# Kernel optimization log

Measured on AMD Instinct MI355X. Metric: run time of the kernel, lower is better.

Reference implementation:

```python
import jax, jax.numpy as jnp
import numpy as np

B, C, H, W = 64, 96, 56, 56
KS = 7
HIDDEN = 512
EPS = 1e-5


def setup_inputs() -> dict:
    key = jax.random.key(0)
    k1, k2, k3 = jax.random.split(key, 3)
    hw = H * W
    return {
        "x": jax.random.normal(k1, (B, C, H, W), dtype=jnp.float32),
        "ln_gamma": jnp.ones((hw,), jnp.float32),
        "ln_beta": jnp.zeros((hw,), jnp.float32),
        "w0": jax.random.normal(k2, (hw, HIDDEN), jnp.float32) * 0.02,
        "b0": jnp.zeros((HIDDEN,), jnp.float32),
        "w1": jax.random.normal(k3, (HIDDEN, KS * KS), jnp.float32) * 0.02,
        "b1": jnp.zeros((KS * KS,), jnp.float32),
        "attn_bias": jnp.zeros((B * C,), jnp.float32),
    }


def reference(x, ln_gamma, ln_beta, w0, b0, w1, b1, attn_bias):
    b, c, h, w = x.shape
    a = x.reshape(b, c, h * w)  # B C (HW)
    # LayerNorm over flattened spatial dim
    mu = jnp.mean(a, axis=-1, keepdims=True)
    var = jnp.mean(jnp.square(a - mu), axis=-1, keepdims=True)
    a = (a - mu) * jax.lax.rsqrt(var + EPS) * ln_gamma + ln_beta
    # 2-layer MLP -> per-(B,C) KxK kernel; exact GELU matches torch nn.GELU()
    a = jax.nn.gelu(jnp.einsum("bcn,nd->bcd", a, w0) + b0, approximate=False)
    a = jnp.einsum("bcd,dk->bck", a, w1) + b1  # (B, C, K*K)
    weight = a.reshape(b * c, 1, KS, KS)  # OIHW, one input channel per group
    xin = x.reshape(1, b * c, h, w)
    pad = KS // 2
    out = jax.lax.conv_general_dilated(
        xin, weight,
        window_strides=(1, 1),
        padding=[(pad, pad), (pad, pad)],
        dimension_numbers=("NCHW", "OIHW", "NCHW"),
        feature_group_count=b * c,
    )
    out = out + attn_bias.reshape(1, b * c, 1, 1)
    return out.reshape(b, c, h, w)
```

## Files before the change

### kernel.cpp

```cpp
#include <hip/hip_runtime.h>
#include <hip/hip_bf16.h>

#define BB 64
#define CC 96
#define HH 56
#define WW 56
#define HWS 3136
#define BC 6144
#define HIDDEN 512
#define KS 7
#define KK2 49
#define K1 3136
#define N1 512
#define EPS 1e-5f

typedef __attribute__((ext_vector_type(8))) short short8;
typedef __attribute__((ext_vector_type(4))) float f32x4;

static __device__ __forceinline__ unsigned short f2bf(float f) {
    union { float f; unsigned int u; } un; un.f = f;
    unsigned int r = un.u + 0x7fffu + ((un.u >> 16) & 1u);
    return (unsigned short)(r >> 16);
}

__global__ __launch_bounds__(256) void ln_kernel(const float* __restrict__ x,
                                                 const float* __restrict__ gamma,
                                                 const float* __restrict__ beta,
                                                 unsigned short* __restrict__ a) {
    const int row = blockIdx.x;
    const float4* xr = (const float4*)(x + (size_t)row * HWS);
    float sum = 0.f, sq = 0.f;
    for (int i = threadIdx.x; i < HWS / 4; i += 256) {
        float4 v = xr[i];
        sum += (v.x + v.y) + (v.z + v.w);
        sq = fmaf(v.x, v.x, sq); sq = fmaf(v.y, v.y, sq);
        sq = fmaf(v.z, v.z, sq); sq = fmaf(v.w, v.w, sq);
    }
    #pragma unroll
    for (int off = 32; off > 0; off >>= 1) {
        sum += __shfl_down(sum, off, 64);
        sq  += __shfl_down(sq,  off, 64);
    }
    __shared__ float s1[4], s2[4];
    const int lane = threadIdx.x & 63, wave = threadIdx.x >> 6;
    if (lane == 0) { s1[wave] = sum; s2[wave] = sq; }
    __syncthreads();
    sum = s1[0] + s1[1] + s1[2] + s1[3];
    sq  = s2[0] + s2[1] + s2[2] + s2[3];
    const float mu = sum * (1.f / HWS);
    const float var = fmaf(-mu, mu, sq * (1.f / HWS));
    const float rs = rsqrtf(var + EPS);
    const float4* gr = (const float4*)gamma;
    const float4* br = (const float4*)beta;
    ushort4* ar = (ushort4*)(a + (size_t)row * HWS);
    for (int i = threadIdx.x; i < HWS / 4; i += 256) {
        float4 v = xr[i], g = gr[i], b = br[i];
        ushort4 o;
        o.x = f2bf((v.x - mu) * rs * g.x + b.x);
        o.y = f2bf((v.y - mu) * rs * g.y + b.y);
        o.z = f2bf((v.z - mu) * rs * g.z + b.z);
        o.w = f2bf((v.w - mu) * rs * g.w + b.w);
        ar[i] = o;
    }
}

__global__ __launch_bounds__(256) void w0t_kernel(const float* __restrict__ w0,
                                                  unsigned short* __restrict__ w0t) {
    __shared__ float tile[64][65];
    const int kb = blockIdx.x * 64;
    const int nb = blockIdx.y * 64;
    for (int i = threadIdx.x; i < 64 * 64; i += 256) {
        int r = i >> 6, c = i & 63;
        tile[r][c] = w0[(size_t)(kb + r) * N1 + nb + c];
    }
    __syncthreads();
    for (int i = threadIdx.x; i < 64 * 64; i += 256) {
        int r = i >> 6, c = i & 63;
        w0t[(size_t)(nb + r) * K1 + kb + c] = f2bf(tile[c][r]);
    }
}

__global__ __launch_bounds__(256) void gemm1_kernel(const unsigned short* __restrict__ A,
                                                    const unsigned short* __restrict__ Bt,
                                                    const float* __restrict__ b0,
                                                    float* __restrict__ hidden) {
    __shared__ __align__(16) char smem[32768];
    const int t = threadIdx.x;
    const int wave = t >> 6, lane = t & 63;
    const int wm = wave >> 1, wn = wave & 1;
    const int tm = blockIdx.x * 64;
    const int tn = blockIdx.y * 64;

    f32x4 acc[2][2] = {};

    auto stage = [&](int buf, int k0) {
        #pragma unroll
        for (int it = 0; it < 2; ++it) {
            int chunk = it * 256 + t;
            int row = chunk >> 3;
            int cb = (chunk & 7) << 4;
            int sb = cb ^ ((row & 7) << 4);
            const char* gA = (const char*)(A + (size_t)(tm + row) * K1 + k0) + sb;
            const char* gB = (const char*)(Bt + (size_t)(tn + row) * K1 + k0) + sb;
            char* ldsA = smem + buf * 16384 + it * 4096 + wave * 1024;
            char* ldsB = smem + buf * 16384 + 8192 + it * 4096 + wave * 1024;
            __builtin_amdgcn_global_load_lds(
                (const __attribute__((address_space(1))) unsigned int*)gA,
                (__attribute__((address_space(3))) unsigned int*)ldsA, 16, 0, 0);
            __builtin_amdgcn_global_load_lds(
                (const __attribute__((address_space(1))) unsigned int*)gB,
                (__attribute__((address_space(3))) unsigned int*)ldsB, 16, 0, 0);
        }
    };

    auto compute = [&](int buf) {
        const char* base = smem + buf * 16384;
        #pragma unroll
        for (int kk = 0; kk < 2; ++kk) {
            short8 af[2], bfr[2];
            const int kbase = kk * 64 + ((lane >> 4) << 4);
            #pragma unroll
            for (int i = 0; i < 2; ++i) {
                int row = wm * 32 + i * 16 + (lane & 15);
                af[i] = *(const short8*)(base + row * 128 + (kbase ^ ((row & 7) << 4)));
            }
            #pragma unroll
            for (int j = 0; j < 2; ++j) {
                int row = wn * 32 + j * 16 + (lane & 15);
                bfr[j] = *(const short8*)(base + 8192 + row * 128 + (kbase ^ ((row & 7) << 4)));
            }
            #pragma unroll
            for (int i = 0; i < 2; ++i)
                #pragma unroll
                for (int j = 0; j < 2; ++j)
                    acc[i][j] = __builtin_amdgcn_mfma_f32_16x16x32_bf16(af[i], bfr[j], acc[i][j], 0, 0, 0);
        }
    };

    stage(0, 0);
    __syncthreads();
    int buf = 0;
    for (int ks = 0; ks < 48; ++ks) {
        stage(buf ^ 1, (ks + 1) * 64);
        compute(buf);
        __syncthreads();
        buf ^= 1;
    }
    compute(buf);

    #pragma unroll
    for (int j = 0; j < 2; ++j) {
        const int gc = tn + wn * 32 + j * 16 + (lane & 15);
        const float bias = b0[gc];
        #pragma unroll
        for (int i = 0; i < 2; ++i) {
            #pragma unroll
            for (int r = 0; r < 4; ++r) {
                int gr = tm + wm * 32 + i * 16 + ((lane >> 4) << 2) + r;
                float v = acc[i][j][r] + bias;
                float g = 0.5f * v * (1.0f + erff(v * 0.70710678118f));
                hidden[(size_t)gr * N1 + gc] = g;
            }
        }
    }
}

__global__ __launch_bounds__(256) void gemm2_kernel(const float* __restrict__ hidden,
                                                    const float* __restrict__ w1,
                                                    const float* __restrict__ b1,
                                                    float* __restrict__ kw) {
    __shared__ float hs[4][HIDDEN];
    const int row0 = blockIdx.x * 4;
    for (int i = threadIdx.x; i < (4 * HIDDEN) / 4; i += 256)
        ((float4*)hs)[i] = ((const float4*)(hidden + (size_t)row0 * HIDDEN))[i];
    __syncthreads();
    const int wrow = threadIdx.x >> 6, lane = threadIdx.x & 63;
    const int n = lane < KK2 ? lane : KK2 - 1;
    float acc = 0.f;
    #pragma unroll 8
    for (int k = 0; k < HIDDEN; ++k)
        acc = fmaf(hs[wrow][k], w1[k * KK2 + n], acc);
    if (lane < KK2)
        kw[(size_t)(row0 + wrow) * KK2 + lane] = acc + b1[lane];
}

#define TSTRIDE 68
#define TFLOATS (62 * TSTRIDE)
__global__ __launch_bounds__(256) void conv_kernel(const float* __restrict__ x,
                                                   const float* __restrict__ kw,
                                                   const float* __restrict__ attn_bias,
                                                   float* __restrict__ out) {
    __shared__ __align__(16) float tile[2][TFLOATS];
    __shared__ __align__(16) float wsm[2][52];
    const int t = threadIdx.x;
    const int plane0 = blockIdx.x * 2;
    const float* xp = x + (size_t)plane0 * HWS;

    if (t < 98) {
        int p = t / 49, j = t % 49;
        wsm[p][j] = kw[(size_t)(plane0 + p) * KK2 + j];
    }
    for (int i = t; i < 2108; i += 256) {
        int p = i / 1054;
        int rem = i - p * 1054;
        int r = rem / 17;
        int c4 = (rem - r * 17) * 4;
        const float* xpp = xp + p * HWS;
        int sr = r - 3;
        float4 v;
        float* vc = (float*)&v;
        #pragma unroll
        for (int j = 0; j < 4; ++j) {
            int sc = c4 + j - 3;
            vc[j] = (sr >= 0 && sr < HH && sc >= 0 && sc < WW) ? xpp[sr * WW + sc] : 0.f;
        }
        *(float4*)&tile[p][r * TSTRIDE + c4] = v;
    }
    __syncthreads();

    if (t < 224) {
        const int p = t / 112;
        const int idx = t - p * 112;
        const int tr = idx / 14;
        const int tc = idx - tr * 14;
        const int plane = plane0 + p;
        const int c0 = tc * 4;

        float wr[49];
        #pragma unroll
        for (int i = 0; i < 12; ++i) {
            float4 v = *(const float4*)&wsm[p][4 * i];
            wr[4 * i] = v.x; wr[4 * i + 1] = v.y; wr[4 * i + 2] = v.z; wr[4 * i + 3] = v.w;
        }
        wr[48] = wsm[p][48];

        const float bias = attn_bias[plane];
        float acc[7][4];
        #pragma unroll
        for (int o = 0; o < 7; ++o)
            #pragma unroll
            for (int j = 0; j < 4; ++j) acc[o][j] = bias;

        const float* tp = &tile[p][tr * 7 * TSTRIDE + c0];
        #pragma unroll
        for (int ir = 0; ir < 13; ++ir) {
            float rv[10];
            float4 va = *(const float4*)(tp + ir * TSTRIDE);
            float4 vb = *(const float4*)(tp + ir * TSTRIDE + 4);
            float2 vc2 = *(const float2*)(tp + ir * TSTRIDE + 8);
            rv[0] = va.x; rv[1] = va.y; rv[2] = va.z; rv[3] = va.w;
            rv[4] = vb.x; rv[5] = vb.y; rv[6] = vb.z; rv[7] = vb.w;
            rv[8] = vc2.x; rv[9] = vc2.y;
            #pragma unroll
            for (int kr = 0; kr < 7; ++kr) {
                const int o = ir - kr;
                if (o >= 0 && o < 7) {
                    #pragma unroll
                    for (int dc = 0; dc < 7; ++dc) {
                        float wv = wr[kr * 7 + dc];
                        acc[o][0] = fmaf(rv[dc],     wv, acc[o][0]);
                        acc[o][1] = fmaf(rv[dc + 1], wv, acc[o][1]);
                        acc[o][2] = fmaf(rv[dc + 2], wv, acc[o][2]);
                        acc[o][3] = fmaf(rv[dc + 3], wv, acc[o][3]);
                    }
                }
            }
        }
        float* op = out + (size_t)plane * HWS + tr * 7 * WW + c0;
        #pragma unroll
        for (int o = 0; o < 7; ++o) {
            float4 v = { acc[o][0], acc[o][1], acc[o][2], acc[o][3] };
            *(float4*)(op + o * WW) = v;
        }
    }
}

extern "C" void kernel_launch(void* const* d_in, const int* in_sizes, int n_in,
                              void* d_out, int out_size, void* d_ws, size_t ws_size,
                              hipStream_t stream) {
    const float* x        = (const float*)d_in[0];
    const float* ln_g     = (const float*)d_in[1];
    const float* ln_b     = (const float*)d_in[2];
    const float* w0       = (const float*)d_in[3];
    const float* b0       = (const float*)d_in[4];
    const float* w1       = (const float*)d_in[5];
    const float* b1       = (const float*)d_in[6];
    const float* attn_b   = (const float*)d_in[7];
    float* out = (float*)d_out;

    char* ws = (char*)d_ws;
    unsigned short* a_bf  = (unsigned short*)ws;
    unsigned short* w0t   = (unsigned short*)(ws + 38535168);
    float*          hidden = (float*)(ws + 41746432);
    float*          kw     = (float*)(ws + 54329344);

    hipLaunchKernelGGL(ln_kernel,    dim3(BC),     dim3(256), 0, stream, x, ln_g, ln_b, a_bf);
    hipLaunchKernelGGL(w0t_kernel,   dim3(49, 8),  dim3(256), 0, stream, w0, w0t);
    hipLaunchKernelGGL(gemm1_kernel, dim3(96, 8),  dim3(256), 0, stream, a_bf, w0t, b0, hidden);
    hipLaunchKernelGGL(gemm2_kernel, dim3(BC / 4), dim3(256), 0, stream, hidden, w1, b1, kw);
    hipLaunchKernelGGL(conv_kernel,  dim3(BC / 2), dim3(256), 0, stream, x, kw, attn_b, out);
}
```

Measured before the change: 272.4 us.

## Store hidden activations as bf16 and widen conv per-thread output tile

The GELU output of the first GEMM is now written as bf16 instead of fp32, which halves that intermediate's traffic, and the second GEMM reads it as bf16 with four independent accumulators. Separately, the depthwise conv kernel now runs 128-thread blocks where each thread computes an 8-wide by 7-row output tile instead of 4-wide, so each loaded input row feeds more FMAs. The cost is extra rounding error in the hidden activations, higher register pressure in the conv, and fewer threads per block to stage the tile.

```diff
diff --git a/kernel.cpp b/kernel.cpp
--- a/kernel.cpp
+++ b/kernel.cpp
@@ -21,6 +21,10 @@
     union { float f; unsigned int u; } un; un.f = f;
     unsigned int r = un.u + 0x7fffu + ((un.u >> 16) & 1u);
     return (unsigned short)(r >> 16);
+}
+static __device__ __forceinline__ float bf2f(unsigned short u) {
+    union { unsigned int u; float f; } un; un.u = ((unsigned int)u) << 16;
+    return un.f;
 }
 
 __global__ __launch_bounds__(256) void ln_kernel(const float* __restrict__ x,
@@ -83,7 +87,7 @@
 __global__ __launch_bounds__(256) void gemm1_kernel(const unsigned short* __restrict__ A,
                                                     const unsigned short* __restrict__ Bt,
                                                     const float* __restrict__ b0,
-                                                    float* __restrict__ hidden) {
+                                                    unsigned short* __restrict__ hidden) {
     __shared__ __align__(16) char smem[32768];
     const int t = threadIdx.x;
     const int wave = t >> 6, lane = t & 63;
@@ -159,34 +163,40 @@
                 int gr = tm + wm * 32 + i * 16 + ((lane >> 4) << 2) + r;
                 float v = acc[i][j][r] + bias;
                 float g = 0.5f * v * (1.0f + erff(v * 0.70710678118f));
-                hidden[(size_t)gr * N1 + gc] = g;
+                hidden[(size_t)gr * N1 + gc] = f2bf(g);
             }
         }
     }
 }
 
-__global__ __launch_bounds__(256) void gemm2_kernel(const float* __restrict__ hidden,
+__global__ __launch_bounds__(256) void gemm2_kernel(const unsigned short* __restrict__ hidden,
                                                     const float* __restrict__ w1,
                                                     const float* __restrict__ b1,
                                                     float* __restrict__ kw) {
-    __shared__ float hs[4][HIDDEN];
+    __shared__ unsigned short hs[4][HIDDEN];
     const int row0 = blockIdx.x * 4;
-    for (int i = threadIdx.x; i < (4 * HIDDEN) / 4; i += 256)
-        ((float4*)hs)[i] = ((const float4*)(hidden + (size_t)row0 * HIDDEN))[i];
+    if (threadIdx.x < 256) {
+        ((short8*)hs)[threadIdx.x] = ((const short8*)(hidden + (size_t)row0 * HIDDEN))[threadIdx.x];
+    }
     __syncthreads();
     const int wrow = threadIdx.x >> 6, lane = threadIdx.x & 63;
     const int n = lane < KK2 ? lane : KK2 - 1;
-    float acc = 0.f;
-    #pragma unroll 8
-    for (int k = 0; k < HIDDEN; ++k)
-        acc = fmaf(hs[wrow][k], w1[k * KK2 + n], acc);
+    float a0 = 0.f, a1 = 0.f, a2 = 0.f, a3 = 0.f;
+    #pragma unroll 4
+    for (int k = 0; k < HIDDEN; k += 4) {
+        ushort4 h4 = *(const ushort4*)&hs[wrow][k];
+        a0 = fmaf(bf2f(h4.x), w1[(k    ) * KK2 + n], a0);
+        a1 = fmaf(bf2f(h4.y), w1[(k + 1) * KK2 + n], a1);
+        a2 = fmaf(bf2f(h4.z), w1[(k + 2) * KK2 + n], a2);
+        a3 = fmaf(bf2f(h4.w), w1[(k + 3) * KK2 + n], a3);
+    }
     if (lane < KK2)
-        kw[(size_t)(row0 + wrow) * KK2 + lane] = acc + b1[lane];
+        kw[(size_t)(row0 + wrow) * KK2 + lane] = (a0 + a1) + (a2 + a3) + b1[lane];
 }
 
 #define TSTRIDE 68
 #define TFLOATS (62 * TSTRIDE)
-__global__ __launch_bounds__(256) void conv_kernel(const float* __restrict__ x,
+__global__ __launch_bounds__(128) void conv_kernel(const float* __restrict__ x,
                                                    const float* __restrict__ kw,
                                                    const float* __restrict__ attn_bias,
                                                    float* __restrict__ out) {
@@ -200,7 +210,7 @@
         int p = t / 49, j = t % 49;
         wsm[p][j] = kw[(size_t)(plane0 + p) * KK2 + j];
     }
-    for (int i = t; i < 2108; i += 256) {
+    for (int i = t; i < 2108; i += 128) {
         int p = i / 1054;
         int rem = i - p * 1054;
         int r = rem / 17;
@@ -218,13 +228,13 @@
     }
     __syncthreads();
 
-    if (t < 224) {
-        const int p = t / 112;
-        const int idx = t - p * 112;
-        const int tr = idx / 14;
-        const int tc = idx - tr * 14;
+    if (t < 112) {
+        const int p = t / 56;
+        const int rem = t - p * 56;
+        const int tr = rem / 7;
+        const int tc = rem - tr * 7;
         const int plane = plane0 + p;
-        const int c0 = tc * 4;
+        const int c0 = tc * 8;
 
         float wr[49];
         #pragma unroll
@@ -235,33 +245,34 @@
         wr[48] = wsm[p][48];
 
         const float bias = attn_bias[plane];
-        float acc[7][4];
+        float acc[7][8];
         #pragma unroll
         for (int o = 0; o < 7; ++o)
             #pragma unroll
-            for (int j = 0; j < 4; ++j) acc[o][j] = bias;
+            for (int j = 0; j < 8; ++j) acc[o][j] = bias;
 
         const float* tp = &tile[p][tr * 7 * TSTRIDE + c0];
         #pragma unroll
         for (int ir = 0; ir < 13; ++ir) {
-            float rv[10];
+            float rv[14];
             float4 va = *(const float4*)(tp + ir * TSTRIDE);
             float4 vb = *(const float4*)(tp + ir * TSTRIDE + 4);
-            float2 vc2 = *(const float2*)(tp + ir * TSTRIDE + 8);
-            rv[0] = va.x; rv[1] = va.y; rv[2] = va.z; rv[3] = va.w;
-            rv[4] = vb.x; rv[5] = vb.y; rv[6] = vb.z; rv[7] = vb.w;
-            rv[8] = vc2.x; rv[9] = vc2.y;
+            float4 vc4 = *(const float4*)(tp + ir * TSTRIDE + 8);
+            float2 vd = *(const float2*)(tp + ir * TSTRIDE + 12);
+            rv[0] = va.x;  rv[1] = va.y;  rv[2] = va.z;  rv[3] = va.w;
+            rv[4] = vb.x;  rv[5] = vb.y;  rv[6] = vb.z;  rv[7] = vb.w;
+            rv[8] = vc4.x; rv[9] = vc4.y; rv[10] = vc4.z; rv[11] = vc4.w;
+            rv[12] = vd.x; rv[13] = vd.y;
             #pragma unroll
             for (int kr = 0; kr < 7; ++kr) {
                 const int o = ir - kr;
                 if (o >= 0 && o < 7) {
                     #pragma unroll
                     for (int dc = 0; dc < 7; ++dc) {
-                        float wv = wr[kr * 7 + dc];
-                        acc[o][0] = fmaf(rv[dc],     wv, acc[o][0]);
-                        acc[o][1] = fmaf(rv[dc + 1], wv, acc[o][1]);
-                        acc[o][2] = fmaf(rv[dc + 2], wv, acc[o][2]);
-                        acc[o][3] = fmaf(rv[dc + 3], wv, acc[o][3]);
+                        const float wv = wr[kr * 7 + dc];
+                        #pragma unroll
+                        for (int j = 0; j < 8; ++j)
+                            acc[o][j] = fmaf(rv[dc + j], wv, acc[o][j]);
                     }
                 }
             }
@@ -269,8 +280,10 @@
         float* op = out + (size_t)plane * HWS + tr * 7 * WW + c0;
         #pragma unroll
         for (int o = 0; o < 7; ++o) {
-            float4 v = { acc[o][0], acc[o][1], acc[o][2], acc[o][3] };
-            *(float4*)(op + o * WW) = v;
+            float4 v0 = { acc[o][0], acc[o][1], acc[o][2], acc[o][3] };
+            float4 v1 = { acc[o][4], acc[o][5], acc[o][6], acc[o][7] };
+            *(float4*)(op + o * WW) = v0;
+            *(float4*)(op + o * WW + 4) = v1;
         }
     }
 }
@@ -289,14 +302,14 @@
     float* out = (float*)d_out;
 
     char* ws = (char*)d_ws;
-    unsigned short* a_bf  = (unsigned short*)ws;
-    unsigned short* w0t   = (unsigned short*)(ws + 38535168);
-    float*          hidden = (float*)(ws + 41746432);
-    float*          kw     = (float*)(ws + 54329344);
+    unsigned short* a_bf   = (unsigned short*)ws;
+    unsigned short* w0t    = (unsigned short*)(ws + 38535168);
+    unsigned short* hidden = (unsigned short*)(ws + 41746432);
+    float*          kw     = (float*)(ws + 48037888);
 
     hipLaunchKernelGGL(ln_kernel,    dim3(BC),     dim3(256), 0, stream, x, ln_g, ln_b, a_bf);
     hipLaunchKernelGGL(w0t_kernel,   dim3(49, 8),  dim3(256), 0, stream, w0, w0t);
     hipLaunchKernelGGL(gemm1_kernel, dim3(96, 8),  dim3(256), 0, stream, a_bf, w0t, b0, hidden);
     hipLaunchKernelGGL(gemm2_kernel, dim3(BC / 4), dim3(256), 0, stream, hidden, w1, b1, kw);
-    hipLaunchKernelGGL(conv_kernel,  dim3(BC / 2), dim3(256), 0, stream, x, kw, attn_b, out);
-}
+    hipLaunchKernelGGL(conv_kernel,  dim3(BC / 2), dim3(128), 0, stream, x, kw, attn_b, out);
+}
```

Result: no change. 273.1 us (+0.3%).
